# Kernel tuning notes

Hardware: AMD Instinct MI355X
Metric: run time of the kernel (lower is better)

Reference implementation:

```python
import jax, jax.numpy as jnp
import numpy as np

NUM_HEADS = 16
HEAD_DIM = 64  # latent_dim // num_heads = 1024 // 16


def setup_inputs() -> dict:
    key = jax.random.key(0)
    k1, k2, k3, k4 = jax.random.split(key, 4)
    B, S, C = 4, 2048, 1024
    x = jax.random.normal(k1, (B, S, C), dtype=jnp.float32)
    # torch nn.Linear weight layout: [out_features, in_features]
    W_qkv = jax.random.normal(k2, (2 * 1024 + C, C), dtype=jnp.float32) * (C ** -0.5)
    W_out = jax.random.normal(k3, (C, C), dtype=jnp.float32) * (C ** -0.5)
    b_out = jax.random.normal(k4, (C,), dtype=jnp.float32) * 0.01
    return {"x": x, "W_qkv": W_qkv, "W_out": W_out, "b_out": b_out}


def reference(x, W_qkv, W_out, b_out):
    B, S, C = x.shape
    H, CH = NUM_HEADS, HEAD_DIM
    qkv = jnp.einsum('bsc,oc->bso', x, W_qkv)          # [B, S, 2*latent + C]
    qkv = qkv.reshape(B, S, H, -1)                      # per-head: [CH, CH, C//H]
    q = qkv[..., :CH]
    k = qkv[..., CH:2 * CH]
    v = qkv[..., 2 * CH:]
    energy = jnp.einsum('bqhc,bkhc->bhqk', q, k)        # full score matrix
    scale = jnp.asarray(C, x.dtype) ** 0.5              # note: original scales by sqrt(C), not sqrt(head_dim)
    attn = jax.nn.softmax(energy / scale, axis=-1)
    out = jnp.einsum('bhqk,bkhc->bqhc', attn, v).reshape(B, S, -1)
    out = jnp.einsum('bsc,oc->bso', out, W_out) + b_out
    return out + x
```

## Files before the change

### kernel.cpp

```cpp
#include <hip/hip_runtime.h>
#include <hip/hip_bf16.h>
#include <stdint.h>

#define BB 4
#define SS 2048
#define CC 1024
#define HH 16
#define DD 64
#define MTOT (BB*SS)
#define NQKV 3072

typedef __attribute__((ext_vector_type(8))) short short8;
typedef __attribute__((ext_vector_type(4))) float f32x4;

#define MFMA16(A,B,C) __builtin_amdgcn_mfma_f32_16x16x32_bf16((A),(B),(C),0,0,0)
#define BARRIER() asm volatile("s_barrier" ::: "memory")

__device__ __forceinline__ ushort f2bf(float f) {
  uint32_t u = __builtin_bit_cast(uint32_t, f);
  u += 0x7FFFu + ((u >> 16) & 1u);
  return (ushort)(u >> 16);
}

__device__ __forceinline__ float bf2f(ushort u) {
  return __builtin_bit_cast(float, (uint32_t)u << 16);
}

__device__ __forceinline__ unsigned cvtpk(float lo, float hi) {
  unsigned r;
  asm("v_cvt_pk_bf16_f32 %0, %1, %2" : "=v"(r) : "v"(lo), "v"(hi));
  return r;
}

__device__ __forceinline__ float hw_exp2(float x) {
  float r;
  asm("v_exp_f32 %0, %1" : "=v"(r) : "v"(x));
  return r;
}

__global__ void cvt3_kernel(const float* __restrict__ a, ushort* __restrict__ da, int na4,
                            const float* __restrict__ b, ushort* __restrict__ db, int nb4,
                            const float* __restrict__ c, ushort* __restrict__ dc, int nc4) {
  int total = na4 + nb4 + nc4;
  int stride = gridDim.x * blockDim.x;
  for (int i = blockIdx.x * blockDim.x + threadIdx.x; i < total; i += stride) {
    const float4* s; ushort4* d; int k;
    if (i < na4)            { s = (const float4*)a; d = (ushort4*)da; k = i; }
    else if (i < na4 + nb4) { s = (const float4*)b; d = (ushort4*)db; k = i - na4; }
    else                    { s = (const float4*)c; d = (ushort4*)dc; k = i - na4 - nb4; }
    float4 v = s[k];
    ushort4 o;
    o.x = f2bf(v.x); o.y = f2bf(v.y); o.z = f2bf(v.z); o.w = f2bf(v.w);
    d[k] = o;
  }
}

__device__ __forceinline__ void stage_half128(const ushort* __restrict__ gsrc, ushort* ldsbase, int tid) {
  #pragma unroll
  for (int ld = 0; ld < 4; ++ld) {
    int ci = ld * 256 + tid;
    int row = ci >> 3, slot = ci & 7;
    const ushort* src = gsrc + (size_t)row * 1024 + ((slot ^ (row & 7)) << 3);
    __builtin_amdgcn_global_load_lds(
        (const __attribute__((address_space(1))) uint32_t*)src,
        (__attribute__((address_space(3))) uint32_t*)(ldsbase + ci * 8), 16, 0, 0);
  }
}

__device__ __forceinline__ short8 rd_frag(const ushort* Lb, int row, int slot) {
  return *(const short8*)(Lb + row * 64 + ((slot ^ (row & 7)) << 3));
}

__device__ __forceinline__ void core128(const ushort* __restrict__ A, const ushort* __restrict__ Bw,
                                        int m0, int n0, ushort* L, f32x4 acc[4][4]) {
  const int tid = threadIdx.x, lane = tid & 63, w = tid >> 6;
  const int q = lane & 15, g = lane >> 4;
  const int wm = (w >> 1) * 64, wn = (w & 1) * 64;
  const ushort* Ag = A + (size_t)m0 * 1024;
  const ushort* Bg = Bw + (size_t)n0 * 1024;

  #pragma unroll
  for (int tt = 0; tt < 2; ++tt) {
    stage_half128(Ag + tt * 64, L + tt * 16384, tid);
    stage_half128(Bg + tt * 64, L + tt * 16384 + 8192, tid);
  }
  asm volatile("s_waitcnt vmcnt(8)" ::: "memory");
  BARRIER();

  #pragma unroll 1
  for (int t = 0; t < 16; ++t) {
    const ushort* La = L + (t & 1) * 16384;
    const ushort* Lb = La + 8192;
    short8 af[4][2], bf[4][2];
    #pragma unroll
    for (int mi = 0; mi < 4; ++mi)
      #pragma unroll
      for (int ks = 0; ks < 2; ++ks)
        af[mi][ks] = rd_frag(La, wm + mi * 16 + q, ks * 4 + g);
    #pragma unroll
    for (int nj = 0; nj < 4; ++nj)
      #pragma unroll
      for (int ks = 0; ks < 2; ++ks)
        bf[nj][ks] = rd_frag(Lb, wn + nj * 16 + q, ks * 4 + g);
    #pragma unroll
    for (int mi = 0; mi < 4; ++mi)
      #pragma unroll
      for (int nj = 0; nj < 4; ++nj) {
        acc[mi][nj] = MFMA16(af[mi][0], bf[nj][0], acc[mi][nj]);
        acc[mi][nj] = MFMA16(af[mi][1], bf[nj][1], acc[mi][nj]);
      }
    BARRIER();
    if (t <= 13) {
      ushort* Ls = L + (t & 1) * 16384;
      stage_half128(Ag + (t + 2) * 64, Ls, tid);
      stage_half128(Bg + (t + 2) * 64, Ls + 8192, tid);
      asm volatile("s_waitcnt vmcnt(8)" ::: "memory");
      BARRIER();
    } else if (t == 14) {
      asm volatile("s_waitcnt vmcnt(0)" ::: "memory");
      BARRIER();
    }
  }
}

__global__ __launch_bounds__(256, 2) void gemm_qkv(const ushort* __restrict__ xb, const ushort* __restrict__ wqkv,
                                                   ushort* __restrict__ qfbuf, ushort* __restrict__ kfbuf,
                                                   ushort* __restrict__ vfbuf) {
  __shared__ __align__(16) ushort L[32768];
  const int bid = blockIdx.x;
  const int xcd = bid & 7, r0 = bid >> 3;
  const int m0 = (r0 / 3) * 128, n0 = (xcd * 3 + (r0 % 3)) * 128;

  f32x4 acc[4][4];
  #pragma unroll
  for (int i = 0; i < 4; ++i)
    #pragma unroll
    for (int j = 0; j < 4; ++j) acc[i][j] = f32x4{0.f, 0.f, 0.f, 0.f};
  core128(xb, wqkv, m0, n0, L, acc);

  const int lane = threadIdx.x & 63, wave = threadIdx.x >> 6;
  const int g = lane >> 4, q = lane & 15;
  const int wm = (wave >> 1) * 64, wn = (wave & 1) * 64;
  const int s0 = m0 & 2047, bb = m0 >> 11;

  #pragma unroll
  for (int j = 0; j < 4; ++j) {
    int n = n0 + wn + j * 16 + q;
    int h = n / 192;
    int which = (n - h * 192) >> 6;
    float scl = (which == 0) ? 0.045084222f : 1.0f;
    int nc = wn + j * 16 + q;
    #pragma unroll
    for (int i = 0; i < 4; ++i) {
      #pragma unroll
      for (int rr = 0; rr < 4; ++rr) {
        int mr = wm + i * 16 + g * 4 + rr;
        L[mr * 128 + (nc ^ ((mr & 7) << 4))] = f2bf(acc[i][j][rr] * scl);
      }
    }
  }
  __syncthreads();

  {
    const int n_g = n0 + wave * 32;
    const int h = n_g / 192, rem = n_g - h * 192, which = rem >> 6;
    const int bh = bb * 16 + h;
    if (which < 2) {
      ushort* dst0 = (which == 0) ? qfbuf : kfbuf;
      const int c0 = (rem & 63) >> 5;
      #pragma unroll
      for (int k = 0; k < 8; ++k) {
        int jt = (s0 >> 4) + k;
        int mr = k * 16 + (lane & 15);
        int nc0 = wave * 32 + (lane >> 4) * 8;
        short8 v = *(const short8*)(L + mr * 128 + (nc0 ^ ((mr & 7) << 4)));
        *(short8*)(dst0 + ((((size_t)bh * 128 + jt) * 2 + c0) * 64 + lane) * 8) = v;
      }
    } else {
      const int ct0 = (rem & 63) >> 4;
      #pragma unroll
      for (int k = 0; k < 8; ++k) {
        int jcr = k >> 1, ct = ct0 + (k & 1);
        int nc = wave * 32 + (k & 1) * 16 + (lane & 15);
        int mrb = jcr * 32 + (lane >> 4) * 8;
        short8 v;
        #pragma unroll
        for (int e = 0; e < 8; ++e) {
          int mr = mrb + e;
          v[e] = (short)L[mr * 128 + (nc ^ ((mr & 7) << 4))];
        }
        int jc = (s0 >> 5) + jcr;
        *(short8*)(vfbuf + ((((size_t)bh * 64 + jc) * 4 + ct) * 64 + lane) * 8) = v;
      }
    }
  }
}

__global__ __launch_bounds__(256, 2) void gemm_out(const ushort* __restrict__ ab, const ushort* __restrict__ wout,
                                                   const ushort* __restrict__ xbb, const float* __restrict__ bias,
                                                   float* __restrict__ out) {
  __shared__ __align__(16) ushort L[32768];
  const int bid = blockIdx.x;
  const int sw = (bid & 7) * 64 + (bid >> 3);
  const int m0 = (sw & 63) * 128, n0 = (sw >> 6) * 128;

  f32x4 acc[4][4];
  #pragma unroll
  for (int i = 0; i < 4; ++i)
    #pragma unroll
    for (int j = 0; j < 4; ++j) acc[i][j] = f32x4{0.f, 0.f, 0.f, 0.f};
  core128(ab, wout, m0, n0, L, acc);

  const int tid = threadIdx.x;
  const int lane = tid & 63, wave = tid >> 6;
  const int g = lane >> 4, q = lane & 15;
  const int wm = (wave >> 1) * 64, wn = (wave & 1) * 64;
  float* Lf = reinterpret_cast<float*>(L);

  #pragma unroll
  for (int j = 0; j < 4; ++j) {
    int nc = wn + j * 16 + q;
    #pragma unroll
    for (int i = 0; i < 4; ++i) {
      #pragma unroll
      for (int rr = 0; rr < 4; ++rr) {
        int mr = wm + i * 16 + g * 4 + rr;
        int swz = ((mr & 4) << 0) | ((mr & 8) << 1);
        Lf[mr * 128 + (nc ^ swz)] = acc[i][j][rr];
      }
    }
  }
  __syncthreads();

  #pragma unroll
  for (int k = 0; k < 16; ++k) {
    int ci = k * 256 + tid;
    int row = ci >> 5, cb = (ci & 31) * 4;
    int swz = ((row & 4) << 0) | ((row & 8) << 1);
    float4 v = *(const float4*)(Lf + row * 128 + (cb ^ swz));
    size_t m = (size_t)(m0 + row);
    int n = n0 + cb;
    ushort4 xr = *(const ushort4*)(xbb + m * 1024 + n);
    float4 bv = *(const float4*)(bias + n);
    float4 o;
    o.x = v.x + bv.x + bf2f(xr.x);
    o.y = v.y + bv.y + bf2f(xr.y);
    o.z = v.z + bv.z + bf2f(xr.z);
    o.w = v.w + bv.w + bf2f(xr.w);
    *(float4*)(out + m * 1024 + n) = o;
  }
}

__device__ __forceinline__ void attn_step(const short8 kf[4][2], const short8 vf[2][4],
                                          const short8 qf[2][2], const short8 onesf,
                                          f32x4 oa[2][4], f32x4 la[2],
                                          ushort* pw0, int g, int q) {
  const f32x4 zed = {0.f, 0.f, 0.f, 0.f};
  #pragma unroll
  for (int t = 0; t < 2; ++t) {
    f32x4 sa[4];
    __builtin_amdgcn_s_setprio(1);
    #pragma unroll
    for (int jt = 0; jt < 4; ++jt) {
      sa[jt] = MFMA16(kf[jt][0], qf[t][0], zed);
      sa[jt] = MFMA16(kf[jt][1], qf[t][1], sa[jt]);
    }
    __builtin_amdgcn_s_setprio(0);
    ushort* pw = pw0 + t * 1152;
    #pragma unroll
    for (int jt = 0; jt < 4; ++jt) {
      uint2 wv;
      wv.x = cvtpk(hw_exp2(sa[jt][0]), hw_exp2(sa[jt][1]));
      wv.y = cvtpk(hw_exp2(sa[jt][2]), hw_exp2(sa[jt][3]));
      *reinterpret_cast<uint2*>(pw + q * 72 + jt * 16 + 4 * g) = wv;
    }
    #pragma unroll
    for (int jc = 0; jc < 2; ++jc) {
      short8 pa = *reinterpret_cast<const short8*>(pw + q * 72 + jc * 32 + g * 8);
      __builtin_amdgcn_s_setprio(1);
      #pragma unroll
      for (int ct = 0; ct < 4; ++ct)
        oa[t][ct] = MFMA16(pa, vf[jc][ct], oa[t][ct]);
      la[t] = MFMA16(pa, onesf, la[t]);
      __builtin_amdgcn_s_setprio(0);
    }
  }
}

__global__ __launch_bounds__(256) void attn_kernel(const ushort* __restrict__ QF, const ushort* __restrict__ KF,
                                                   const ushort* __restrict__ VF, ushort* __restrict__ aout) {
  __shared__ ushort Ps[4][2][16 * 72];
  const int bid = blockIdx.x;
  const int xcd = bid & 7, rr = bid >> 3;
  const int qb = rr & 15, bh = xcd + (rr >> 4) * 8;
  const int lane = threadIdx.x & 63, wave = threadIdx.x >> 6;
  const int g = lane >> 4, q = lane & 15;
  const int qt0 = (qb * 4 + wave) * 2;
  const f32x4 zed = {0.f, 0.f, 0.f, 0.f};

  const ushort* Qb = QF + (size_t)bh * 131072 + lane * 8;
  const ushort* Kp = KF + (size_t)bh * 131072 + lane * 8;
  const ushort* Vp = VF + (size_t)bh * 131072 + lane * 8;
  ushort* pw0 = Ps[wave][0];

  short8 onesf;
  #pragma unroll
  for (int e = 0; e < 8; ++e) onesf[e] = (short)0x3F80;

  short8 qf[2][2];
  #pragma unroll
  for (int t = 0; t < 2; ++t)
    #pragma unroll
    for (int c0 = 0; c0 < 2; ++c0)
      qf[t][c0] = *(const short8*)(Qb + ((size_t)(qt0 + t) * 2 + c0) * 512);

  f32x4 oa[2][4], la[2];
  #pragma unroll
  for (int t = 0; t < 2; ++t) {
    la[t] = zed;
    #pragma unroll
    for (int ct = 0; ct < 4; ++ct) oa[t][ct] = zed;
  }

  short8 kfA[4][2], kfB[4][2], vfA[2][4], vfB[2][4];
  #pragma unroll
  for (int jt = 0; jt < 4; ++jt)
    #pragma unroll
    for (int c0 = 0; c0 < 2; ++c0)
      kfA[jt][c0] = *(const short8*)(Kp + ((size_t)jt * 2 + c0) * 512);

  #pragma unroll 1
  for (int i = 0; i < 32; i += 2) {
    #pragma unroll
    for (int jc = 0; jc < 2; ++jc)
      #pragma unroll
      for (int ct = 0; ct < 4; ++ct)
        vfA[jc][ct] = *(const short8*)(Vp + ((size_t)jc * 4 + ct) * 512);
    #pragma unroll
    for (int jt = 0; jt < 4; ++jt)
      #pragma unroll
      for (int c0 = 0; c0 < 2; ++c0)
        kfB[jt][c0] = *(const short8*)(Kp + 4096 + ((size_t)jt * 2 + c0) * 512);

    attn_step(kfA, vfA, qf, onesf, oa, la, pw0, g, q);

    #pragma unroll
    for (int jc = 0; jc < 2; ++jc)
      #pragma unroll
      for (int ct = 0; ct < 4; ++ct)
        vfB[jc][ct] = *(const short8*)(Vp + 4096 + ((size_t)jc * 4 + ct) * 512);
    if (i + 2 < 32) {
      #pragma unroll
      for (int jt = 0; jt < 4; ++jt)
        #pragma unroll
        for (int c0 = 0; c0 < 2; ++c0)
          kfA[jt][c0] = *(const short8*)(Kp + 8192 + ((size_t)jt * 2 + c0) * 512);
    }

    attn_step(kfB, vfB, qf, onesf, oa, la, pw0, g, q);

    Kp += 8192; Vp += 8192;
  }

  const int b = bh >> 4, h = bh & 15;
  #pragma unroll
  for (int t = 0; t < 2; ++t) {
    float inv[4];
    #pragma unroll
    for (int r2 = 0; r2 < 4; ++r2) inv[r2] = 1.0f / la[t][r2];
    #pragma unroll
    for (int ct = 0; ct < 4; ++ct) {
      size_t rowb = (size_t)b * SS + (qt0 + t) * 16 + 4 * g;
      int col = h * DD + ct * 16 + q;
      aout[(rowb + 0) * CC + col] = f2bf(oa[t][ct][0] * inv[0]);
      aout[(rowb + 1) * CC + col] = f2bf(oa[t][ct][1] * inv[1]);
      aout[(rowb + 2) * CC + col] = f2bf(oa[t][ct][2] * inv[2]);
      aout[(rowb + 3) * CC + col] = f2bf(oa[t][ct][3] * inv[3]);
    }
  }
}

extern "C" void kernel_launch(void* const* d_in, const int* in_sizes, int n_in,
                              void* d_out, int out_size, void* d_ws, size_t ws_size,
                              hipStream_t stream) {
  const float* x    = (const float*)d_in[0];
  const float* wqkv = (const float*)d_in[1];
  const float* wout = (const float*)d_in[2];
  const float* bias = (const float*)d_in[3];
  float* out = (float*)d_out;

  ushort* xb    = (ushort*)d_ws;
  ushort* wqkvb = xb + (size_t)8 * 1024 * 1024;
  ushort* woutb = wqkvb + (size_t)3 * 1024 * 1024;
  ushort* qfbuf = woutb + (size_t)1024 * 1024;
  ushort* kfbuf = qfbuf + (size_t)8 * 1024 * 1024;
  ushort* vfbuf = kfbuf + (size_t)8 * 1024 * 1024;
  ushort* aout  = vfbuf + (size_t)8 * 1024 * 1024;

  hipLaunchKernelGGL(cvt3_kernel, dim3(2048), dim3(256), 0, stream,
                     x, xb, 8 * 1024 * 1024 / 4,
                     wqkv, wqkvb, 3 * 1024 * 1024 / 4,
                     wout, woutb, 1024 * 1024 / 4);

  hipLaunchKernelGGL(gemm_qkv, dim3(1536), dim3(256), 0, stream,
                     xb, wqkvb, qfbuf, kfbuf, vfbuf);
  hipLaunchKernelGGL(attn_kernel, dim3(1024), dim3(256), 0, stream,
                     qfbuf, kfbuf, vfbuf, aout);
  hipLaunchKernelGGL(gemm_out, dim3(512), dim3(256), 0, stream,
                     aout, woutb, xb, bias, out);
}
```

Before: 190.9 us.

## Shrink attention tiles to one query tile per wave and drop K/V double buffering

Each wave in the attention kernel now handles a single 16-row query tile instead of two, and the grid doubles to 2048 blocks. The explicit register double-buffering of K/V fragments is replaced by a simple loop that loads 32 keys per iteration and uses half the shared-memory P buffer. The aim is lower register use and higher occupancy or wave parallelism, at the cost of reading K and V twice as often per query row and losing the manual load/compute overlap.

```diff
diff --git a/kernel.cpp b/kernel.cpp
--- a/kernel.cpp
+++ b/kernel.cpp
@@ -251,132 +251,85 @@
   }
 }
 
-__device__ __forceinline__ void attn_step(const short8 kf[4][2], const short8 vf[2][4],
-                                          const short8 qf[2][2], const short8 onesf,
-                                          f32x4 oa[2][4], f32x4 la[2],
-                                          ushort* pw0, int g, int q) {
-  const f32x4 zed = {0.f, 0.f, 0.f, 0.f};
-  #pragma unroll
-  for (int t = 0; t < 2; ++t) {
-    f32x4 sa[4];
-    __builtin_amdgcn_s_setprio(1);
-    #pragma unroll
-    for (int jt = 0; jt < 4; ++jt) {
-      sa[jt] = MFMA16(kf[jt][0], qf[t][0], zed);
-      sa[jt] = MFMA16(kf[jt][1], qf[t][1], sa[jt]);
-    }
-    __builtin_amdgcn_s_setprio(0);
-    ushort* pw = pw0 + t * 1152;
-    #pragma unroll
-    for (int jt = 0; jt < 4; ++jt) {
-      uint2 wv;
-      wv.x = cvtpk(hw_exp2(sa[jt][0]), hw_exp2(sa[jt][1]));
-      wv.y = cvtpk(hw_exp2(sa[jt][2]), hw_exp2(sa[jt][3]));
-      *reinterpret_cast<uint2*>(pw + q * 72 + jt * 16 + 4 * g) = wv;
-    }
-    #pragma unroll
-    for (int jc = 0; jc < 2; ++jc) {
-      short8 pa = *reinterpret_cast<const short8*>(pw + q * 72 + jc * 32 + g * 8);
-      __builtin_amdgcn_s_setprio(1);
-      #pragma unroll
-      for (int ct = 0; ct < 4; ++ct)
-        oa[t][ct] = MFMA16(pa, vf[jc][ct], oa[t][ct]);
-      la[t] = MFMA16(pa, onesf, la[t]);
-      __builtin_amdgcn_s_setprio(0);
-    }
-  }
-}
-
 __global__ __launch_bounds__(256) void attn_kernel(const ushort* __restrict__ QF, const ushort* __restrict__ KF,
                                                    const ushort* __restrict__ VF, ushort* __restrict__ aout) {
-  __shared__ ushort Ps[4][2][16 * 72];
+  __shared__ ushort Ps[4][16 * 72];
   const int bid = blockIdx.x;
-  const int xcd = bid & 7, rr = bid >> 3;
-  const int qb = rr & 15, bh = xcd + (rr >> 4) * 8;
+  const int xcd = bid & 7, r = bid >> 3;
+  const int qb = r & 31, bh = xcd + (r >> 5) * 8;
   const int lane = threadIdx.x & 63, wave = threadIdx.x >> 6;
   const int g = lane >> 4, q = lane & 15;
-  const int qt0 = (qb * 4 + wave) * 2;
+  const int qt = qb * 4 + wave;
   const f32x4 zed = {0.f, 0.f, 0.f, 0.f};
 
   const ushort* Qb = QF + (size_t)bh * 131072 + lane * 8;
   const ushort* Kp = KF + (size_t)bh * 131072 + lane * 8;
   const ushort* Vp = VF + (size_t)bh * 131072 + lane * 8;
-  ushort* pw0 = Ps[wave][0];
+  ushort* pw = Ps[wave];
 
   short8 onesf;
   #pragma unroll
   for (int e = 0; e < 8; ++e) onesf[e] = (short)0x3F80;
 
-  short8 qf[2][2];
-  #pragma unroll
-  for (int t = 0; t < 2; ++t)
-    #pragma unroll
-    for (int c0 = 0; c0 < 2; ++c0)
-      qf[t][c0] = *(const short8*)(Qb + ((size_t)(qt0 + t) * 2 + c0) * 512);
-
-  f32x4 oa[2][4], la[2];
-  #pragma unroll
-  for (int t = 0; t < 2; ++t) {
-    la[t] = zed;
-    #pragma unroll
-    for (int ct = 0; ct < 4; ++ct) oa[t][ct] = zed;
-  }
-
-  short8 kfA[4][2], kfB[4][2], vfA[2][4], vfB[2][4];
-  #pragma unroll
-  for (int jt = 0; jt < 4; ++jt)
-    #pragma unroll
-    for (int c0 = 0; c0 < 2; ++c0)
-      kfA[jt][c0] = *(const short8*)(Kp + ((size_t)jt * 2 + c0) * 512);
+  short8 qf[2];
+  #pragma unroll
+  for (int c0 = 0; c0 < 2; ++c0)
+    qf[c0] = *(const short8*)(Qb + ((size_t)qt * 2 + c0) * 512);
+
+  f32x4 oa[4], la;
+  la = zed;
+  #pragma unroll
+  for (int ct = 0; ct < 4; ++ct) oa[ct] = zed;
 
   #pragma unroll 1
-  for (int i = 0; i < 32; i += 2) {
-    #pragma unroll
-    for (int jc = 0; jc < 2; ++jc)
-      #pragma unroll
-      for (int ct = 0; ct < 4; ++ct)
-        vfA[jc][ct] = *(const short8*)(Vp + ((size_t)jc * 4 + ct) * 512);
-    #pragma unroll
-    for (int jt = 0; jt < 4; ++jt)
+  for (int j0 = 0; j0 < SS; j0 += 32) {
+    const int jt0 = j0 >> 4, jc = j0 >> 5;
+    short8 kf[2][2], vf[4];
+    #pragma unroll
+    for (int jj = 0; jj < 2; ++jj)
       #pragma unroll
       for (int c0 = 0; c0 < 2; ++c0)
-        kfB[jt][c0] = *(const short8*)(Kp + 4096 + ((size_t)jt * 2 + c0) * 512);
-
-    attn_step(kfA, vfA, qf, onesf, oa, la, pw0, g, q);
-
-    #pragma unroll
-    for (int jc = 0; jc < 2; ++jc)
-      #pragma unroll
-      for (int ct = 0; ct < 4; ++ct)
-        vfB[jc][ct] = *(const short8*)(Vp + 4096 + ((size_t)jc * 4 + ct) * 512);
-    if (i + 2 < 32) {
-      #pragma unroll
-      for (int jt = 0; jt < 4; ++jt)
-        #pragma unroll
-        for (int c0 = 0; c0 < 2; ++c0)
-          kfA[jt][c0] = *(const short8*)(Kp + 8192 + ((size_t)jt * 2 + c0) * 512);
-    }
-
-    attn_step(kfB, vfB, qf, onesf, oa, la, pw0, g, q);
-
-    Kp += 8192; Vp += 8192;
+        kf[jj][c0] = *(const short8*)(Kp + ((size_t)(jt0 + jj) * 2 + c0) * 512);
+    #pragma unroll
+    for (int ct = 0; ct < 4; ++ct)
+      vf[ct] = *(const short8*)(Vp + ((size_t)jc * 4 + ct) * 512);
+
+    f32x4 sa[2];
+    __builtin_amdgcn_s_setprio(1);
+    #pragma unroll
+    for (int jj = 0; jj < 2; ++jj) {
+      sa[jj] = MFMA16(kf[jj][0], qf[0], zed);
+      sa[jj] = MFMA16(kf[jj][1], qf[1], sa[jj]);
+    }
+    __builtin_amdgcn_s_setprio(0);
+    #pragma unroll
+    for (int jj = 0; jj < 2; ++jj) {
+      uint2 wv;
+      wv.x = cvtpk(hw_exp2(sa[jj][0]), hw_exp2(sa[jj][1]));
+      wv.y = cvtpk(hw_exp2(sa[jj][2]), hw_exp2(sa[jj][3]));
+      *reinterpret_cast<uint2*>(pw + q * 72 + jj * 16 + 4 * g) = wv;
+    }
+    short8 pa = *reinterpret_cast<const short8*>(pw + q * 72 + g * 8);
+    __builtin_amdgcn_s_setprio(1);
+    #pragma unroll
+    for (int ct = 0; ct < 4; ++ct)
+      oa[ct] = MFMA16(pa, vf[ct], oa[ct]);
+    la = MFMA16(pa, onesf, la);
+    __builtin_amdgcn_s_setprio(0);
   }
 
   const int b = bh >> 4, h = bh & 15;
-  #pragma unroll
-  for (int t = 0; t < 2; ++t) {
-    float inv[4];
-    #pragma unroll
-    for (int r2 = 0; r2 < 4; ++r2) inv[r2] = 1.0f / la[t][r2];
-    #pragma unroll
-    for (int ct = 0; ct < 4; ++ct) {
-      size_t rowb = (size_t)b * SS + (qt0 + t) * 16 + 4 * g;
-      int col = h * DD + ct * 16 + q;
-      aout[(rowb + 0) * CC + col] = f2bf(oa[t][ct][0] * inv[0]);
-      aout[(rowb + 1) * CC + col] = f2bf(oa[t][ct][1] * inv[1]);
-      aout[(rowb + 2) * CC + col] = f2bf(oa[t][ct][2] * inv[2]);
-      aout[(rowb + 3) * CC + col] = f2bf(oa[t][ct][3] * inv[3]);
-    }
+  float inv[4];
+  #pragma unroll
+  for (int r2 = 0; r2 < 4; ++r2) inv[r2] = 1.0f / la[r2];
+  #pragma unroll
+  for (int ct = 0; ct < 4; ++ct) {
+    size_t rowb = (size_t)b * SS + qt * 16 + 4 * g;
+    int col = h * DD + ct * 16 + q;
+    aout[(rowb + 0) * CC + col] = f2bf(oa[ct][0] * inv[0]);
+    aout[(rowb + 1) * CC + col] = f2bf(oa[ct][1] * inv[1]);
+    aout[(rowb + 2) * CC + col] = f2bf(oa[ct][2] * inv[2]);
+    aout[(rowb + 3) * CC + col] = f2bf(oa[ct][3] * inv[3]);
   }
 }
 
@@ -404,7 +357,7 @@
 
   hipLaunchKernelGGL(gemm_qkv, dim3(1536), dim3(256), 0, stream,
                      xb, wqkvb, qfbuf, kfbuf, vfbuf);
-  hipLaunchKernelGGL(attn_kernel, dim3(1024), dim3(256), 0, stream,
+  hipLaunchKernelGGL(attn_kernel, dim3(2048), dim3(256), 0, stream,
                      qfbuf, kfbuf, vfbuf, aout);
   hipLaunchKernelGGL(gemm_out, dim3(512), dim3(256), 0, stream,
                      aout, woutb, xb, bias, out);
```

Result: slower. 222.1 us (+16.4%).
